# Kernel tuning notes

Measured on AMD Instinct MI355X. Metric: run time of the kernel, lower is better.

Reference implementation:

```python
import jax, jax.numpy as jnp
import numpy as np

N, M, FDIM, EDIM, H, HEADS = 8192, 8192, 128, 128, 64, 4
NEG = -1e9


def setup_inputs() -> dict:
    key = jax.random.key(0)
    ks = jax.random.split(key, 6)
    F0 = jax.random.normal(ks[0], (N, FDIM), dtype=jnp.float32)
    E0 = jax.random.normal(ks[1], (M, EDIM), dtype=jnp.float32)
    A = jax.random.randint(ks[2], (N, M), 0, 2, dtype=jnp.int32)
    Wf = jax.random.normal(ks[3], (HEADS, FDIM, H), dtype=jnp.float32) * 0.05
    We = jax.random.normal(ks[4], (HEADS, EDIM, H), dtype=jnp.float32) * 0.05
    a = jax.random.normal(ks[5], (HEADS, H), dtype=jnp.float32) * 0.05
    return {"F0": F0, "E0": E0, "A": A, "Wf": Wf, "We": We, "a": a}


def reference(F0, E0, A, Wf, We, a):
    # Per-head linear projections: h=head, n/m=nodes, d=hidden
    F1 = jnp.einsum('nf,hfd->hnd', F0, Wf)   # [H, N, D]
    E1 = jnp.einsum('me,hed->hmd', E0, We)   # [H, M, D]
    # Additive GAT scores: (h_src @ a) + (h_dst @ a), broadcast over the grid
    e_src = jnp.einsum('hnd,hd->hn', F1, a)  # [H, N]
    e_dst = jnp.einsum('hmd,hd->hm', E1, a)  # [H, M]
    e = jax.nn.leaky_relu(e_src[:, :, None] + e_dst[:, None, :], negative_slope=0.2)
    e = jnp.where(A[None, :, :] > 0, e, NEG)
    alpha = jax.nn.softmax(e, axis=-1)       # [H, N, M]
    h_prime = jnp.einsum('hnm,hmd->hnd', alpha, E1)  # [H, N, D]
    out = jnp.mean(h_prime, axis=0)          # mean over heads -> [N, D]
    return jax.nn.softmax(out, axis=-1)
```

## Files before the change

### kernel.cpp

```cpp
#include <hip/hip_runtime.h>
#include <hip/hip_fp16.h>

#define NN 8192
#define MM 8192
#define FD 128
#define EDm 128
#define HD 64
#define NH 4

#define MSPLIT 4
#define MRANGE (MM / MSPLIT)
#define MSTEP 128
#define NITER (MRANGE / MSTEP)
#define NTILE 32

typedef float f32x4 __attribute__((ext_vector_type(4)));
typedef _Float16 h16x8 __attribute__((ext_vector_type(8)));
typedef _Float16 h16x4 __attribute__((ext_vector_type(4)));
typedef int i32x4 __attribute__((ext_vector_type(4)));
typedef unsigned int u32;

__global__ void k_vf(const float* __restrict__ Wf, const float* __restrict__ a,
                     float* __restrict__ vf) {
  int t = threadIdx.x;
  int h = t >> 7, f = t & 127;
  const float* w = Wf + (size_t)(h * FD + f) * HD;
  const float* av = a + h * HD;
  float s = 0.f;
#pragma unroll
  for (int d = 0; d < HD; ++d) s += w[d] * av[d];
  vf[h * FD + f] = s;
}

__global__ void k_esrc(const float* __restrict__ F0, const float* __restrict__ vf,
                       float* __restrict__ esrc) {
  int t = blockIdx.x * blockDim.x + threadIdx.x;
  int n = t >> 2, h = t & 3;
  const float4* fr = (const float4*)(F0 + (size_t)n * FD);
  const float4* vr = (const float4*)(vf + h * FD);
  float s = 0.f;
#pragma unroll
  for (int i = 0; i < FD / 4; ++i) {
    float4 x = fr[i], y = vr[i];
    s += x.x * y.x + x.y * y.y + x.z * y.z + x.w * y.w;
  }
  esrc[h * NN + n] = s;
}

__global__ void k_e1(const float* __restrict__ E0, const float* __restrict__ We,
                     const float* __restrict__ a, _Float16* __restrict__ E1T,
                     _Float16* __restrict__ edh, _Float16* __restrict__ ed2h) {
  int wid = (blockIdx.x * blockDim.x + threadIdx.x) >> 6;
  int lane = threadIdx.x & 63;
  int h = wid >> 11;
  int mg = wid & 2047;
  int m = mg * 4;
  const float* we = We + (size_t)h * EDm * HD + lane;
  const float* e0r = E0 + (size_t)m * EDm;
  float a0 = 0.f, a1 = 0.f, a2 = 0.f, a3 = 0.f;
#pragma unroll 4
  for (int e = 0; e < EDm; ++e) {
    float wv = we[e * HD];
    a0 += e0r[e] * wv;
    a1 += e0r[EDm + e] * wv;
    a2 += e0r[2 * EDm + e] * wv;
    a3 += e0r[3 * EDm + e] * wv;
  }
  h16x4 hv = {(_Float16)a0, (_Float16)a1, (_Float16)a2, (_Float16)a3};
  *(h16x4*)(E1T + (size_t)(h * HD + lane) * MM + m) = hv;
  float av = a[h * HD + lane];
  float d0 = a0 * av, d1 = a1 * av, d2 = a2 * av, d3 = a3 * av;
#pragma unroll
  for (int o = 32; o; o >>= 1) {
    d0 += __shfl_xor(d0, o);
    d1 += __shfl_xor(d1, o);
    d2 += __shfl_xor(d2, o);
    d3 += __shfl_xor(d3, o);
  }
  if (lane == 0) {
    const float L2E = 1.4426950408889634f;
    edh[h * MM + m + 0] = (_Float16)exp2f(d0 * L2E);
    edh[h * MM + m + 1] = (_Float16)exp2f(d1 * L2E);
    edh[h * MM + m + 2] = (_Float16)exp2f(d2 * L2E);
    edh[h * MM + m + 3] = (_Float16)exp2f(d3 * L2E);
    ed2h[h * MM + m + 0] = (_Float16)exp2f(0.2f * d0 * L2E);
    ed2h[h * MM + m + 1] = (_Float16)exp2f(0.2f * d1 * L2E);
    ed2h[h * MM + m + 2] = (_Float16)exp2f(0.2f * d2 * L2E);
    ed2h[h * MM + m + 3] = (_Float16)exp2f(0.2f * d3 * L2E);
  }
}

__device__ __forceinline__ uint2 packmask(i32x4 a) {
  uint2 r;
  r.x = (a.x > 0 ? 0xffffu : 0u) | (a.y > 0 ? 0xffff0000u : 0u);
  r.y = (a.z > 0 ? 0xffffu : 0u) | (a.w > 0 ? 0xffff0000u : 0u);
  return r;
}

__global__ __launch_bounds__(256) void k_main(
    const int* __restrict__ A, const _Float16* __restrict__ E1T,
    const float* __restrict__ esrc, const _Float16* __restrict__ edh,
    const _Float16* __restrict__ ed2h, float* __restrict__ pnum,
    float* __restrict__ pden) {
  __shared__ __align__(16) char smem[17408];
  u32* Amh = (u32*)smem;
  u32* EdU = (u32*)(smem + 8704);
  float* Hpf = (float*)smem;

  const int t = threadIdx.x;
  const int lane = t & 63;
  const int h = t >> 6;
  const int col = lane & 15;
  const int quad = lane >> 4;

  const int b = blockIdx.x;
  const int xcdr = b & 7;
  const int split = xcdr >> 1;
  const int ntile = ((b >> 3) << 1) | (xcdr & 1);
  const int n0 = ntile * NTILE;
  const int m0 = split * MRANGE;
  const float L2E = 1.4426950408889634f;

  float s0 = esrc[h * NN + n0 + col];
  float s1 = esrc[h * NN + n0 + 16 + col];
  _Float16 e80 = (_Float16)exp2f(0.8f * s0 * L2E);
  _Float16 e81 = (_Float16)exp2f(0.8f * s1 * L2E);
  h16x8 es80 = {e80, e80, e80, e80, e80, e80, e80, e80};
  h16x8 es81 = {e81, e81, e81, e81, e81, e81, e81, e81};

  f32x4 acc[2][4] = {};
  f32x4 accd[2] = {};
  const h16x8 ones = {(_Float16)1.f, (_Float16)1.f, (_Float16)1.f, (_Float16)1.f,
                      (_Float16)1.f, (_Float16)1.f, (_Float16)1.f, (_Float16)1.f};

  const int arow = t >> 3;
  const int achk = t & 7;
  const int* aptr = A + (size_t)(n0 + arow) * MM + m0 + achk * 4;
  u32* amw = Amh + arow * 68 + achk * 2;
  const _Float16* edlane =
      ((lane < 32) ? edh : ed2h) + (size_t)h * MM + m0 + (lane & 31) * 4;
  u32* edw = EdU + h * 136 + ((lane >= 32) ? 68 : 0) + (lane & 31) * 2;

  i32x4 apf[4];
#pragma unroll
  for (int j = 0; j < 4; ++j)
    apf[j] = __builtin_nontemporal_load((const i32x4*)(aptr + 32 * j));
  uint2 edpf = *(const uint2*)edlane;

  const _Float16* bq = E1T + (size_t)(h * HD + col) * MM + m0 + quad * 8;

  for (int it = 0; it < NITER; ++it) {
    const int k0 = it * MSTEP;
#pragma unroll
    for (int j = 0; j < 4; ++j) *(uint2*)(amw + 16 * j) = packmask(apf[j]);
    *(uint2*)edw = edpf;
    __syncthreads();

    h16x8 bfr[16];
#pragma unroll
    for (int dt = 0; dt < 4; ++dt)
#pragma unroll
      for (int kk = 0; kk < 4; ++kk)
        bfr[dt * 4 + kk] =
            *(const h16x8*)(bq + (size_t)dt * 16 * MM + k0 + kk * 32);

    if (it + 1 < NITER) {
#pragma unroll
      for (int j = 0; j < 4; ++j)
        apf[j] = __builtin_nontemporal_load(
            (const i32x4*)(aptr + k0 + MSTEP + 32 * j));
      edpf = *(const uint2*)(edlane + k0 + MSTEP);
    }

#pragma unroll
    for (int kk = 0; kk < 4; ++kk) {
      const int base = kk * 16 + quad * 4;
      uint4 ma = *(const uint4*)(Amh + col * 68 + base);
      uint4 mb = *(const uint4*)(Amh + (col + 16) * 68 + base);
      h16x8 edv = *(const h16x8*)(EdU + h * 136 + base);
      h16x8 e2v = *(const h16x8*)(EdU + h * 136 + 68 + base);
      h16x8 w0 = __builtin_elementwise_max(edv * es80, e2v);
      h16x8 w1 = __builtin_elementwise_max(edv * es81, e2v);
      union { h16x8 v; uint4 u; } a0, a1;
      a0.v = w0; a1.v = w1;
      a0.u.x &= ma.x; a0.u.y &= ma.y; a0.u.z &= ma.z; a0.u.w &= ma.w;
      a1.u.x &= mb.x; a1.u.y &= mb.y; a1.u.z &= mb.z; a1.u.w &= mb.w;
#pragma unroll
      for (int dt = 0; dt < 4; ++dt) {
        acc[0][dt] = __builtin_amdgcn_mfma_f32_16x16x32_f16(a0.v, bfr[dt * 4 + kk],
                                                            acc[0][dt], 0, 0, 0);
        acc[1][dt] = __builtin_amdgcn_mfma_f32_16x16x32_f16(a1.v, bfr[dt * 4 + kk],
                                                            acc[1][dt], 0, 0, 0);
      }
      accd[0] = __builtin_amdgcn_mfma_f32_16x16x32_f16(a0.v, ones, accd[0], 0, 0, 0);
      accd[1] = __builtin_amdgcn_mfma_f32_16x16x32_f16(a1.v, ones, accd[1], 0, 0, 0);
    }
    __syncthreads();
  }

  float* pn = pnum + (size_t)(split * NH + h) * NN * HD;
  float* pd = pden + (size_t)(split * NH + h) * NN;
#pragma unroll
  for (int rt = 0; rt < 2; ++rt) {
#pragma unroll
    for (int dt = 0; dt < 4; ++dt)
#pragma unroll
      for (int r2 = 0; r2 < 4; ++r2)
        Hpf[h * 1088 + (quad * 4 + r2) * 68 + dt * 16 + col] = acc[rt][dt][r2];
    if (col == 0) {
#pragma unroll
      for (int r2 = 0; r2 < 4; ++r2)
        Hpf[h * 1088 + (quad * 4 + r2) * 68 + 64] = accd[rt][r2];
    }
    __syncthreads();
#pragma unroll
    for (int j = 0; j < 4; ++j) {
      int row = j * 4 + (lane >> 4);
      int c4 = lane & 15;
      f32x4 v = *(const f32x4*)(Hpf + h * 1088 + row * 68 + c4 * 4);
      __builtin_nontemporal_store(
          v, (f32x4*)(pn + (size_t)(n0 + rt * 16 + row) * HD + c4 * 4));
    }
    if (lane < 16) pd[n0 + rt * 16 + lane] = Hpf[h * 1088 + lane * 68 + 64];
    __syncthreads();
  }
}

__global__ void k_comb(const float* __restrict__ pnum, const float* __restrict__ pden,
                       float* __restrict__ out) {
  int t = threadIdx.x;
  int lane = t & 63, w = t >> 6;
  int n = blockIdx.x * 4 + w;
  float v = 0.f;
#pragma unroll
  for (int h = 0; h < NH; ++h) {
    float num = 0.f, den = 0.f;
#pragma unroll
    for (int s = 0; s < MSPLIT; ++s) {
      num += pnum[((size_t)(s * NH + h) * NN + n) * HD + lane];
      den += pden[(size_t)(s * NH + h) * NN + n];
    }
    v += num / den;
  }
  v *= 0.25f;
  float mx = v;
#pragma unroll
  for (int o = 32; o; o >>= 1) mx = fmaxf(mx, __shfl_xor(mx, o));
  const float L2E = 1.4426950408889634f;
  float p = exp2f((v - mx) * L2E);
  float sm = p;
#pragma unroll
  for (int o = 32; o; o >>= 1) sm += __shfl_xor(sm, o);
  out[(size_t)n * HD + lane] = p / sm;
}

extern "C" void kernel_launch(void* const* d_in, const int* in_sizes, int n_in,
                              void* d_out, int out_size, void* d_ws, size_t ws_size,
                              hipStream_t stream) {
  const float* F0 = (const float*)d_in[0];
  const float* E0 = (const float*)d_in[1];
  const int* A = (const int*)d_in[2];
  const float* Wf = (const float*)d_in[3];
  const float* We = (const float*)d_in[4];
  const float* a = (const float*)d_in[5];
  float* out = (float*)d_out;

  char* w = (char*)d_ws;
  float* esrc = (float*)w;        w += (size_t)NH * NN * 4;
  _Float16* edh = (_Float16*)w;   w += (size_t)NH * MM * 2;
  _Float16* ed2h = (_Float16*)w;  w += (size_t)NH * MM * 2;
  float* vf = (float*)w;          w += (size_t)NH * FD * 4;
  _Float16* E1T = (_Float16*)w;   w += (size_t)NH * HD * MM * 2;
  float* pnum = (float*)w;        w += (size_t)MSPLIT * NH * NN * HD * 4;
  float* pden = (float*)w;        w += (size_t)MSPLIT * NH * NN * 4;

  k_vf<<<1, 512, 0, stream>>>(Wf, a, vf);
  k_esrc<<<(NH * NN) / 256, 256, 0, stream>>>(F0, vf, esrc);
  k_e1<<<(NH * MM / 4) / 4, 256, 0, stream>>>(E0, We, a, E1T, edh, ed2h);
  k_main<<<256 * MSPLIT, 256, 0, stream>>>(A, E1T, esrc, edh, ed2h, pnum, pden);
  k_comb<<<NN / 4, 256, 0, stream>>>(pnum, pden, out);
}
```

Baseline: 518.4 us.

## Drop LDS staging in main kernel; load mask and weights directly per wave

Removes shared-memory staging of the adjacency mask and edge exponentials, so each wave loads its A rows and ed vectors straight from global memory every 32-column step with no barriers. Each of the four head-waves now reads the same A tile independently, which quadruples A traffic relative to cache, and software prefetching across iterations is gone. It also simplifies mask packing with a multiply trick, drops the XCD-aware block remapping, and writes outputs directly instead of through LDS with nontemporal stores.

```diff
diff --git a/kernel.cpp b/kernel.cpp
--- a/kernel.cpp
+++ b/kernel.cpp
@@ -10,9 +10,6 @@
 
 #define MSPLIT 4
 #define MRANGE (MM / MSPLIT)
-#define MSTEP 128
-#define NITER (MRANGE / MSTEP)
-#define NTILE 32
 
 typedef float f32x4 __attribute__((ext_vector_type(4)));
 typedef _Float16 h16x8 __attribute__((ext_vector_type(8)));
@@ -90,11 +87,8 @@
   }
 }
 
-__device__ __forceinline__ uint2 packmask(i32x4 a) {
-  uint2 r;
-  r.x = (a.x > 0 ? 0xffffu : 0u) | (a.y > 0 ? 0xffff0000u : 0u);
-  r.y = (a.z > 0 ? 0xffffu : 0u) | (a.w > 0 ? 0xffff0000u : 0u);
-  return r;
+__device__ __forceinline__ u32 hm2(int a, int b) {
+  return ((u32)a | ((u32)b << 16)) * 0xffffu;
 }
 
 __global__ __launch_bounds__(256) void k_main(
@@ -102,11 +96,6 @@
     const float* __restrict__ esrc, const _Float16* __restrict__ edh,
     const _Float16* __restrict__ ed2h, float* __restrict__ pnum,
     float* __restrict__ pden) {
-  __shared__ __align__(16) char smem[17408];
-  u32* Amh = (u32*)smem;
-  u32* EdU = (u32*)(smem + 8704);
-  float* Hpf = (float*)smem;
-
   const int t = threadIdx.x;
   const int lane = t & 63;
   const int h = t >> 6;
@@ -114,10 +103,9 @@
   const int quad = lane >> 4;
 
   const int b = blockIdx.x;
-  const int xcdr = b & 7;
-  const int split = xcdr >> 1;
-  const int ntile = ((b >> 3) << 1) | (xcdr & 1);
-  const int n0 = ntile * NTILE;
+  const int split = b & 3;
+  const int ntile = b >> 2;
+  const int n0 = ntile * 32;
   const int m0 = split * MRANGE;
   const float L2E = 1.4426950408889634f;
 
@@ -133,69 +121,46 @@
   const h16x8 ones = {(_Float16)1.f, (_Float16)1.f, (_Float16)1.f, (_Float16)1.f,
                       (_Float16)1.f, (_Float16)1.f, (_Float16)1.f, (_Float16)1.f};
 
-  const int arow = t >> 3;
-  const int achk = t & 7;
-  const int* aptr = A + (size_t)(n0 + arow) * MM + m0 + achk * 4;
-  u32* amw = Amh + arow * 68 + achk * 2;
-  const _Float16* edlane =
-      ((lane < 32) ? edh : ed2h) + (size_t)h * MM + m0 + (lane & 31) * 4;
-  u32* edw = EdU + h * 136 + ((lane >= 32) ? 68 : 0) + (lane & 31) * 2;
-
-  i32x4 apf[4];
-#pragma unroll
-  for (int j = 0; j < 4; ++j)
-    apf[j] = __builtin_nontemporal_load((const i32x4*)(aptr + 32 * j));
-  uint2 edpf = *(const uint2*)edlane;
-
+  const int* ap0 = A + (size_t)(n0 + col) * MM + m0 + quad * 8;
+  const int* ap1 = ap0 + (size_t)16 * MM;
+  const _Float16* edp = edh + (size_t)h * MM + m0 + quad * 8;
+  const _Float16* e2p = ed2h + (size_t)h * MM + m0 + quad * 8;
   const _Float16* bq = E1T + (size_t)(h * HD + col) * MM + m0 + quad * 8;
 
-  for (int it = 0; it < NITER; ++it) {
-    const int k0 = it * MSTEP;
-#pragma unroll
-    for (int j = 0; j < 4; ++j) *(uint2*)(amw + 16 * j) = packmask(apf[j]);
-    *(uint2*)edw = edpf;
-    __syncthreads();
-
-    h16x8 bfr[16];
-#pragma unroll
-    for (int dt = 0; dt < 4; ++dt)
-#pragma unroll
-      for (int kk = 0; kk < 4; ++kk)
-        bfr[dt * 4 + kk] =
-            *(const h16x8*)(bq + (size_t)dt * 16 * MM + k0 + kk * 32);
-
-    if (it + 1 < NITER) {
-#pragma unroll
-      for (int j = 0; j < 4; ++j)
-        apf[j] = __builtin_nontemporal_load(
-            (const i32x4*)(aptr + k0 + MSTEP + 32 * j));
-      edpf = *(const uint2*)(edlane + k0 + MSTEP);
-    }
-
-#pragma unroll
-    for (int kk = 0; kk < 4; ++kk) {
-      const int base = kk * 16 + quad * 4;
-      uint4 ma = *(const uint4*)(Amh + col * 68 + base);
-      uint4 mb = *(const uint4*)(Amh + (col + 16) * 68 + base);
-      h16x8 edv = *(const h16x8*)(EdU + h * 136 + base);
-      h16x8 e2v = *(const h16x8*)(EdU + h * 136 + 68 + base);
-      h16x8 w0 = __builtin_elementwise_max(edv * es80, e2v);
-      h16x8 w1 = __builtin_elementwise_max(edv * es81, e2v);
-      union { h16x8 v; uint4 u; } a0, a1;
-      a0.v = w0; a1.v = w1;
-      a0.u.x &= ma.x; a0.u.y &= ma.y; a0.u.z &= ma.z; a0.u.w &= ma.w;
-      a1.u.x &= mb.x; a1.u.y &= mb.y; a1.u.z &= mb.z; a1.u.w &= mb.w;
-#pragma unroll
-      for (int dt = 0; dt < 4; ++dt) {
-        acc[0][dt] = __builtin_amdgcn_mfma_f32_16x16x32_f16(a0.v, bfr[dt * 4 + kk],
-                                                            acc[0][dt], 0, 0, 0);
-        acc[1][dt] = __builtin_amdgcn_mfma_f32_16x16x32_f16(a1.v, bfr[dt * 4 + kk],
-                                                            acc[1][dt], 0, 0, 0);
-      }
-      accd[0] = __builtin_amdgcn_mfma_f32_16x16x32_f16(a0.v, ones, accd[0], 0, 0, 0);
-      accd[1] = __builtin_amdgcn_mfma_f32_16x16x32_f16(a1.v, ones, accd[1], 0, 0, 0);
-    }
-    __syncthreads();
+  for (int k = 0; k < MRANGE; k += 32) {
+    i32x4 a00 = *(const i32x4*)(ap0 + k);
+    i32x4 a01 = *(const i32x4*)(ap0 + k + 4);
+    i32x4 a10 = *(const i32x4*)(ap1 + k);
+    i32x4 a11 = *(const i32x4*)(ap1 + k + 4);
+    h16x8 edv = *(const h16x8*)(edp + k);
+    h16x8 e2v = *(const h16x8*)(e2p + k);
+    h16x8 bf0 = *(const h16x8*)(bq + k);
+    h16x8 bf1 = *(const h16x8*)(bq + (size_t)16 * MM + k);
+    h16x8 bf2 = *(const h16x8*)(bq + (size_t)32 * MM + k);
+    h16x8 bf3 = *(const h16x8*)(bq + (size_t)48 * MM + k);
+
+    union { h16x8 v; uint4 u; } w0, w1;
+    w0.v = __builtin_elementwise_max(edv * es80, e2v);
+    w1.v = __builtin_elementwise_max(edv * es81, e2v);
+    w0.u.x &= hm2(a00.x, a00.y);
+    w0.u.y &= hm2(a00.z, a00.w);
+    w0.u.z &= hm2(a01.x, a01.y);
+    w0.u.w &= hm2(a01.z, a01.w);
+    w1.u.x &= hm2(a10.x, a10.y);
+    w1.u.y &= hm2(a10.z, a10.w);
+    w1.u.z &= hm2(a11.x, a11.y);
+    w1.u.w &= hm2(a11.z, a11.w);
+
+    acc[0][0] = __builtin_amdgcn_mfma_f32_16x16x32_f16(w0.v, bf0, acc[0][0], 0, 0, 0);
+    acc[1][0] = __builtin_amdgcn_mfma_f32_16x16x32_f16(w1.v, bf0, acc[1][0], 0, 0, 0);
+    acc[0][1] = __builtin_amdgcn_mfma_f32_16x16x32_f16(w0.v, bf1, acc[0][1], 0, 0, 0);
+    acc[1][1] = __builtin_amdgcn_mfma_f32_16x16x32_f16(w1.v, bf1, acc[1][1], 0, 0, 0);
+    acc[0][2] = __builtin_amdgcn_mfma_f32_16x16x32_f16(w0.v, bf2, acc[0][2], 0, 0, 0);
+    acc[1][2] = __builtin_amdgcn_mfma_f32_16x16x32_f16(w1.v, bf2, acc[1][2], 0, 0, 0);
+    acc[0][3] = __builtin_amdgcn_mfma_f32_16x16x32_f16(w0.v, bf3, acc[0][3], 0, 0, 0);
+    acc[1][3] = __builtin_amdgcn_mfma_f32_16x16x32_f16(w1.v, bf3, acc[1][3], 0, 0, 0);
+    accd[0] = __builtin_amdgcn_mfma_f32_16x16x32_f16(w0.v, ones, accd[0], 0, 0, 0);
+    accd[1] = __builtin_amdgcn_mfma_f32_16x16x32_f16(w1.v, ones, accd[1], 0, 0, 0);
   }
 
   float* pn = pnum + (size_t)(split * NH + h) * NN * HD;
@@ -205,24 +170,15 @@
 #pragma unroll
     for (int dt = 0; dt < 4; ++dt)
 #pragma unroll
+      for (int r2 = 0; r2 < 4; ++r2) {
+        int row = n0 + rt * 16 + quad * 4 + r2;
+        pn[(size_t)row * HD + dt * 16 + col] = acc[rt][dt][r2];
+      }
+    if (col == 0) {
+#pragma unroll
       for (int r2 = 0; r2 < 4; ++r2)
-        Hpf[h * 1088 + (quad * 4 + r2) * 68 + dt * 16 + col] = acc[rt][dt][r2];
-    if (col == 0) {
-#pragma unroll
-      for (int r2 = 0; r2 < 4; ++r2)
-        Hpf[h * 1088 + (quad * 4 + r2) * 68 + 64] = accd[rt][r2];
+        pd[n0 + rt * 16 + quad * 4 + r2] = accd[rt][r2];
     }
-    __syncthreads();
-#pragma unroll
-    for (int j = 0; j < 4; ++j) {
-      int row = j * 4 + (lane >> 4);
-      int c4 = lane & 15;
-      f32x4 v = *(const f32x4*)(Hpf + h * 1088 + row * 68 + c4 * 4);
-      __builtin_nontemporal_store(
-          v, (f32x4*)(pn + (size_t)(n0 + rt * 16 + row) * HD + c4 * 4));
-    }
-    if (lane < 16) pd[n0 + rt * 16 + lane] = Hpf[h * 1088 + lane * 68 + 64];
-    __syncthreads();
   }
 }
 
@@ -277,6 +233,6 @@
   k_vf<<<1, 512, 0, stream>>>(Wf, a, vf);
   k_esrc<<<(NH * NN) / 256, 256, 0, stream>>>(F0, vf, esrc);
   k_e1<<<(NH * MM / 4) / 4, 256, 0, stream>>>(E0, We, a, E1T, edh, ed2h);
-  k_main<<<256 * MSPLIT, 256, 0, stream>>>(A, E1T, esrc, edh, ed2h, pnum, pden);
+  k_main<<<(NN / 32) * MSPLIT, 256, 0, stream>>>(A, E1T, esrc, edh, ed2h, pnum, pden);
   k_comb<<<NN / 4, 256, 0, stream>>>(pnum, pden, out);
 }
```

After: 611.0 us. 17.9% more time.
